# Performance work log

Measured on AMD Instinct MI355X. Metric: run time of the kernel, lower is better.

The kernel has to match this reference:

```python
import jax, jax.numpy as jnp
import numpy as np

N = 50000
E = 800000
D = 128
EPS = 1e-5


def setup_inputs() -> dict:
    key = jax.random.key(0)
    ks = jax.random.split(key, 8)
    scale = 1.0 / np.sqrt(D)
    x = jax.random.normal(ks[0], (N, D), dtype=jnp.float32)
    edge_index = jax.random.randint(ks[1], (2, E), 0, N, dtype=jnp.int64)
    return {
        "x": x,
        "edge_index": edge_index,
        "W1l": jax.random.normal(ks[2], (D, D), dtype=jnp.float32) * scale,
        "b1": jnp.zeros((D,), jnp.float32),
        "W1r": jax.random.normal(ks[3], (D, D), dtype=jnp.float32) * scale,
        "g1": jnp.ones((D,), jnp.float32),
        "bt1": jnp.zeros((D,), jnp.float32),
        "W2l": jax.random.normal(ks[4], (D, D), dtype=jnp.float32) * scale,
        "b2": jnp.zeros((D,), jnp.float32),
        "W2r": jax.random.normal(ks[5], (D, D), dtype=jnp.float32) * scale,
        "g2": jnp.ones((D,), jnp.float32),
        "bt2": jnp.zeros((D,), jnp.float32),
    }


def _sage(x, src, dst, Wl, b, Wr):
    # mean aggregation of source features at destination nodes
    agg = jax.ops.segment_sum(x[src], dst, num_segments=N)  # [N, D]
    deg = jax.ops.segment_sum(jnp.ones((E,), x.dtype), dst, num_segments=N)
    agg = agg / jnp.maximum(deg, 1.0)[:, None]
    # PyG SAGEConv: lin_l(agg) + bias + lin_r(x) (root, no bias)
    return agg @ Wl + b + x @ Wr


def _bn(h, g, bt):
    # training-mode batch norm over node dim
    mu = jnp.mean(h, axis=0)
    var = jnp.var(h, axis=0)
    return (h - mu) * (g / jnp.sqrt(var + EPS)) + bt


def reference(x, edge_index, W1l, b1, W1r, g1, bt1, W2l, b2, W2r, g2, bt2):
    src, dst = edge_index[0], edge_index[1]
    h = _sage(x, src, dst, W1l, b1, W1r)
    h = jax.nn.relu(_bn(h, g1, bt1))
    # dropout = identity (eval mode)
    h = _sage(h, src, dst, W2l, b2, W2r)
    h = _bn(h, g2, bt2)
    # residual (in_channels == out_channels -> identity skip)
    return jax.nn.relu(h + x)
```

## Files before the change

### kernel.cpp

```cpp
#include <hip/hip_runtime.h>

typedef unsigned short u16;
typedef unsigned char u8;
typedef __attribute__((ext_vector_type(8))) short short8;
typedef __attribute__((ext_vector_type(2))) float f32x2;
typedef __attribute__((ext_vector_type(4))) float f32x4;
typedef __attribute__((ext_vector_type(4))) int i32x4;
typedef __attribute__((ext_vector_type(2))) int i32x2;
typedef __attribute__((ext_vector_type(4))) unsigned short us4;
typedef __attribute__((ext_vector_type(8))) unsigned short us8;
typedef __attribute__((ext_vector_type(4))) unsigned int u32x4;

#define N_NODES 50000
#define N_EDGES 800000
#define DIM 128
#define NINV (1.0f / 50000.0f)
#define SROW 136
#define NBKT 3125
#define CAP 512
#define SUPN 800
#define NSUP 63
#define SEGCAP 16384

__device__ __forceinline__ float bf2f(u16 u) {
    union { unsigned int i; float f; } v; v.i = ((unsigned int)u) << 16; return v.f;
}
__device__ __forceinline__ u16 f2bf(float f) {
    union { float f; unsigned int i; } v; v.f = f;
    return (u16)((v.i + 0x7FFFu + ((v.i >> 16) & 1u)) >> 16);
}

__global__ __launch_bounds__(256) void k_prep(
        const float* __restrict__ W1l, const float* __restrict__ W1r, u16* __restrict__ Bp1,
        const float* __restrict__ W2l, const float* __restrict__ W2r, u16* __restrict__ Bp2,
        const float* __restrict__ x, u16* __restrict__ xh, u8* __restrict__ xf8,
        const int* __restrict__ esrc, const int* __restrict__ edst,
        int* __restrict__ segCnt, unsigned* __restrict__ segBuf, int splitB) {
    int b = blockIdx.x;
    if (b < 32) {
        const float* Wl = (b < 16) ? W1l : W2l;
        const float* Wr = (b < 16) ? W1r : W2r;
        u16* Bp = (b < 16) ? Bp1 : Bp2;
        int idx = (b & 15) * 256 + threadIdx.x;
        int lane = idx & 63;
        int kc = (idx >> 6) & 7;
        int nt = idx >> 9;
        int q = lane >> 4, nn = lane & 15;
        int col = nt * 16 + nn;
        #pragma unroll
        for (int j = 0; j < 8; ++j) {
            int k = kc * 32 + q * 8 + j;
            float v = (k < 128) ? Wl[k * 128 + col] : Wr[(k - 128) * 128 + col];
            Bp[(long)idx * 8 + j] = f2bf(v);
        }
    } else if (b < 32 + splitB) {
        long i4 = ((long)(b - 32) * 256 + threadIdx.x) * 4;
        f32x4 v = *(const f32x4*)(x + i4);
        us4 h;
        #pragma unroll
        for (int j = 0; j < 4; ++j) h[j] = f2bf(v[j]);
        *(us4*)(xh + i4) = h;
        int p = __builtin_amdgcn_cvt_pk_fp8_f32(v[0], v[1], 0, false);
        p = __builtin_amdgcn_cvt_pk_fp8_f32(v[2], v[3], p, true);
        *(int*)(xf8 + i4) = p;
    } else {
        __shared__ int sHistB[64], sScanB[64], sCurB[64], sBaseB[64];
        __shared__ unsigned sStage[1024];
        __shared__ u8 sBinOf[1024];
        int tid = threadIdx.x;
        int hb = b - 32 - splitB;
        int e4 = hb * 1024 + tid * 4;
        bool val = e4 < N_EDGES;
        if (tid < 64) sHistB[tid] = 0;
        __syncthreads();
        unsigned ent[4]; int bin[4];
        if (val) {
            i32x4 d4 = *(const i32x4*)(edst + e4);
            i32x4 s4 = *(const i32x4*)(esrc + e4);
            #pragma unroll
            for (int j = 0; j < 4; ++j) {
                unsigned dd = (unsigned)d4[j];
                int bi = (int)(dd / 800u);
                bin[j] = bi;
                ent[j] = ((unsigned)s4[j] << 10) | (dd - (unsigned)bi * 800u);
                atomicAdd(&sHistB[bi], 1);
            }
        }
        __syncthreads();
        if (tid == 0) {
            int acc = 0;
            #pragma unroll
            for (int i = 0; i < 64; ++i) { sScanB[i] = acc; sCurB[i] = acc; acc += sHistB[i]; }
        }
        __syncthreads();
        if (val) {
            #pragma unroll
            for (int j = 0; j < 4; ++j) {
                int p = atomicAdd(&sCurB[bin[j]], 1);
                sStage[p] = ent[j];
                sBinOf[p] = (u8)bin[j];
            }
        }
        __syncthreads();
        if (tid < 64) {
            int c = sHistB[tid];
            sBaseB[tid] = c ? atomicAdd(&segCnt[tid << 4], c) : 0;
        }
        __syncthreads();
        int tcount = sScanB[63] + sHistB[63];
        for (int p = tid; p < tcount; p += 256) {
            int bn = sBinOf[p];
            long ofs = (long)sBaseB[bn] + (p - sScanB[bn]);
            if (ofs < SEGCAP)
                segBuf[(long)bn * SEGCAP + ofs] = sStage[p];
        }
    }
}

__global__ __launch_bounds__(512) void k_sort(
        const int* __restrict__ segCnt, const unsigned* __restrict__ segBuf,
        u16* __restrict__ col_srt, u16* __restrict__ hdr) {
    __shared__ int sHist[SUPN], sStart[SUPN], sCur[SUPN];
    int tid = threadIdx.x;
    int s = blockIdx.x;
    int nnodes = N_NODES - s * SUPN; if (nnodes > SUPN) nnodes = SUPN;
    int ngroups = nnodes >> 4;
    int n = segCnt[s << 4]; if (n > SEGCAP) n = SEGCAP;
    for (int i = tid; i < SUPN; i += 512) { sHist[i] = 0; sCur[i] = 0; }
    __syncthreads();
    const unsigned* seg = segBuf + (long)s * SEGCAP;
    unsigned ent[32];
    #pragma unroll
    for (int i = 0; i < 32; ++i) {
        int idx = i * 512 + tid;
        ent[i] = (idx < n) ? seg[idx] : 0xFFFFFFFFu;
    }
    #pragma unroll
    for (int i = 0; i < 32; ++i)
        if (ent[i] != 0xFFFFFFFFu) atomicAdd(&sHist[ent[i] & 1023u], 1);
    __syncthreads();
    if (tid < ngroups) {
        int base = 0;
        int gb = (s * 50 + tid) * 32;
        #pragma unroll
        for (int i = 0; i < 16; ++i) {
            int node = tid * 16 + i;
            int d = sHist[node];
            int st_c = base < CAP ? base : CAP;
            int en_c = base + d < CAP ? base + d : CAP;
            sStart[node] = base;
            hdr[gb + i] = (u16)st_c;
            hdr[gb + 16 + i] = (u16)(en_c - st_c);
            base += d;
        }
    }
    __syncthreads();
    #pragma unroll
    for (int i = 0; i < 32; ++i) {
        unsigned e = ent[i];
        if (e != 0xFFFFFFFFu) {
            int node = (int)(e & 1023u);
            int pos = atomicAdd(&sCur[node], 1);
            int ofs = sStart[node] + pos;
            if (ofs < CAP)
                col_srt[(long)(s * 50 + (node >> 4)) * CAP + ofs] = (u16)(e >> 10);
        }
    }
}

template<int BN>
__device__ __forceinline__ void acc_row16(u32x4 w,
        f32x2 sum2[8], const f32x2 av2[8], const f32x2 ov2[8]) {
    #pragma unroll
    for (int h = 0; h < 4; ++h) {
        f32x2 lo = __builtin_amdgcn_cvt_pk_f32_fp8((int)w[h], false);
        f32x2 hi = __builtin_amdgcn_cvt_pk_f32_fp8((int)w[h], true);
        if (BN) {
            lo = lo * av2[2 * h] + ov2[2 * h];
            hi = hi * av2[2 * h + 1] + ov2[2 * h + 1];
            lo[0] = lo[0] > 0.f ? lo[0] : 0.f;
            lo[1] = lo[1] > 0.f ? lo[1] : 0.f;
            hi[0] = hi[0] > 0.f ? hi[0] : 0.f;
            hi[1] = hi[1] > 0.f ? hi[1] : 0.f;
        }
        sum2[2 * h]     += lo;
        sum2[2 * h + 1] += hi;
    }
}

template<int BN, int W8>
__global__ __launch_bounds__(256) void k_ag(
        const u8* __restrict__ fq, const u16* __restrict__ fh,
        const u16* __restrict__ hdr, const u16* __restrict__ col_srt,
        const u16* __restrict__ Bph, const float* __restrict__ bias,
        const float* __restrict__ statsPrev, const float* __restrict__ gP,
        const float* __restrict__ btP,
        u16* __restrict__ h16, u8* __restrict__ h8, float* __restrict__ stats) {
    __shared__ u16 sA[16 * SROW];
    __shared__ float acS[256];
    __shared__ __align__(16) u16 sIdx[CAP];
    int tid = threadIdx.x;
    long nodebase = (long)blockIdx.x * 16;

    if (tid < 64)
        *(us8*)(sIdx + tid * 8) = *(const us8*)(col_srt + (long)blockIdx.x * CAP + tid * 8);

    if (BN) {
        if (tid < 128) {
            float s = 0.f, qq = 0.f;
            #pragma unroll
            for (int b = 0; b < 8; ++b) {
                s  += statsPrev[b * 512 + tid];
                qq += statsPrev[b * 512 + 256 + tid];
            }
            float mu = s * NINV;
            float var = qq * NINV - mu * mu;
            float a = gP[tid] * rsqrtf(var + 1e-5f);
            acS[tid] = a;
            acS[128 + tid] = btP[tid] - mu * a;
        }
    }
    __syncthreads();

    {
        int grp = tid >> 4;
        int g   = tid & 15;
        int sub = g >> 3;
        int gl  = g & 7;
        int d16 = gl * 16;
        int st  = hdr[blockIdx.x * 32 + grp];
        int deg = hdr[blockIdx.x * 32 + 16 + grp];
        int s = st, e = st + deg;
        f32x2 av2[8], ov2[8];
        if (BN) {
            #pragma unroll
            for (int p = 0; p < 8; ++p) {
                av2[p] = *(const f32x2*)(acS + d16 + 2 * p);
                ov2[p] = *(const f32x2*)(acS + 128 + d16 + 2 * p);
            }
        }
        f32x2 sum2[8];
        #pragma unroll
        for (int p = 0; p < 8; ++p) sum2[p] = (f32x2){0.f, 0.f};
        int j = s + sub;
        for (; j + 6 < e; j += 8) {
            int i0 = sIdx[j], i1 = sIdx[j + 2], i2 = sIdx[j + 4], i3 = sIdx[j + 6];
            u32x4 w0 = *(const u32x4*)(fq + (long)i0 * DIM + d16);
            u32x4 w1 = *(const u32x4*)(fq + (long)i1 * DIM + d16);
            u32x4 w2 = *(const u32x4*)(fq + (long)i2 * DIM + d16);
            u32x4 w3 = *(const u32x4*)(fq + (long)i3 * DIM + d16);
            acc_row16<BN>(w0, sum2, av2, ov2);
            acc_row16<BN>(w1, sum2, av2, ov2);
            acc_row16<BN>(w2, sum2, av2, ov2);
            acc_row16<BN>(w3, sum2, av2, ov2);
        }
        for (; j < e; j += 2) {
            int i0 = sIdx[j];
            u32x4 w0 = *(const u32x4*)(fq + (long)i0 * DIM + d16);
            acc_row16<BN>(w0, sum2, av2, ov2);
        }
        #pragma unroll
        for (int p = 0; p < 8; ++p) {
            sum2[p][0] += __shfl_xor(sum2[p][0], 8);
            sum2[p][1] += __shfl_xor(sum2[p][1], 8);
        }
        if (sub == 0) {
            float dn = (deg > 0) ? 1.f / (float)deg : 1.f;
            us8 r0, r1;
            #pragma unroll
            for (int k = 0; k < 8; ++k) {
                r0[k] = f2bf(sum2[k >> 1][k & 1] * dn);
                r1[k] = f2bf(sum2[4 + (k >> 1)][k & 1] * dn);
            }
            *(us8*)(sA + grp * SROW + d16) = r0;
            *(us8*)(sA + grp * SROW + d16 + 8) = r1;
        }
    }
    __syncthreads();

    int cg = tid >> 6, lane = tid & 63;
    int q = lane >> 4, nn = lane & 15;
    long rc = nodebase + nn;

    short8 ah[8];
    #pragma unroll
    for (int kc = 0; kc < 4; ++kc)
        ah[kc] = *(const short8*)(sA + nn * SROW + kc * 32 + q * 8);
    #pragma unroll
    for (int kc = 0; kc < 4; ++kc) {
        int ko = kc * 32 + q * 8;
        us8 rv = *(const us8*)(fh + rc * DIM + ko);
        short8 t;
        if (BN) {
            #pragma unroll
            for (int j = 0; j < 8; ++j) {
                float v = bf2f(rv[j]) * acS[ko + j] + acS[128 + ko + j];
                t[j] = (short)f2bf(v > 0.f ? v : 0.f);
            }
        } else {
            #pragma unroll
            for (int j = 0; j < 8; ++j) t[j] = (short)rv[j];
        }
        ah[4 + kc] = t;
    }

    f32x4 acc[2];
    acc[0] = (f32x4){0.f, 0.f, 0.f, 0.f};
    acc[1] = (f32x4){0.f, 0.f, 0.f, 0.f};

    #pragma unroll
    for (int kc = 0; kc < 8; ++kc) {
        #pragma unroll
        for (int nt = 0; nt < 2; ++nt) {
            int ntg = cg * 2 + nt;
            short8 bh = *(const short8*)(Bph + (((ntg * 8 + kc) * 64 + lane) << 3));
            acc[nt] = __builtin_amdgcn_mfma_f32_16x16x32_bf16(ah[kc], bh, acc[nt], 0, 0, 0);
        }
    }

    int bank = blockIdx.x & 7;
    #pragma unroll
    for (int nt = 0; nt < 2; ++nt) {
        int col = cg * 32 + nt * 16 + nn;
        float bv = bias[col];
        float ps = 0.f, pq = 0.f;
        #pragma unroll
        for (int r = 0; r < 4; ++r) {
            float v = acc[nt][r] + bv;
            long idx = (nodebase + q * 4 + r) * DIM + col;
            h16[idx] = f2bf(v);
            if (W8) {
                int pb = __builtin_amdgcn_cvt_pk_fp8_f32(v, v, 0, false);
                h8[idx] = (u8)(pb & 0xff);
            }
            ps += v; pq += v * v;
        }
        ps += __shfl_xor(ps, 16);
        ps += __shfl_xor(ps, 32);
        pq += __shfl_xor(pq, 16);
        pq += __shfl_xor(pq, 32);
        if (q == 0) {
            atomicAdd(&stats[bank * 512 + col], ps);
            atomicAdd(&stats[bank * 512 + 256 + col], pq);
        }
    }
}

__global__ __launch_bounds__(256) void k_bn_add_relu(
        const u16* __restrict__ h, const float* __restrict__ stats,
        const float* __restrict__ g, const float* __restrict__ bt,
        const float* __restrict__ x, float* __restrict__ outv) {
    __shared__ float acS[256];
    int tid = threadIdx.x;
    if (tid < 128) {
        float s = 0.f, qq = 0.f;
        #pragma unroll
        for (int b = 0; b < 8; ++b) {
            s  += stats[b * 512 + tid];
            qq += stats[b * 512 + 256 + tid];
        }
        float mu = s * NINV;
        float var = qq * NINV - mu * mu;
        float a = g[tid] * rsqrtf(var + 1e-5f);
        acS[tid] = a;
        acS[128 + tid] = bt[tid] - mu * a;
    }
    __syncthreads();
    long i8 = ((long)blockIdx.x * 256 + tid) * 8;
    int c = (int)(i8 & 127);
    us8 hv = *(const us8*)(h + i8);
    f32x4 x0 = *(const f32x4*)(x + i8);
    f32x4 x1 = *(const f32x4*)(x + i8 + 4);
    f32x4 r0, r1;
    #pragma unroll
    for (int j = 0; j < 4; ++j) {
        float v = bf2f(hv[j]) * acS[c + j] + acS[128 + c + j] + x0[j];
        r0[j] = v > 0.f ? v : 0.f;
        float w = bf2f(hv[4 + j]) * acS[c + 4 + j] + acS[128 + c + 4 + j] + x1[j];
        r1[j] = w > 0.f ? w : 0.f;
    }
    *(f32x4*)(outv + i8) = r0;
    *(f32x4*)(outv + i8 + 4) = r1;
}

extern "C" void kernel_launch(void* const* d_in, const int* in_sizes, int n_in,
                              void* d_out, int out_size, void* d_ws, size_t ws_size,
                              hipStream_t stream) {
    (void)in_sizes; (void)n_in; (void)out_size; (void)ws_size;
    const float* x   = (const float*)d_in[0];
    const int*   ei  = (const int*)d_in[1];
    const float* W1l = (const float*)d_in[2];
    const float* b1  = (const float*)d_in[3];
    const float* W1r = (const float*)d_in[4];
    const float* g1  = (const float*)d_in[5];
    const float* bt1 = (const float*)d_in[6];
    const float* W2l = (const float*)d_in[7];
    const float* b2  = (const float*)d_in[8];
    const float* W2r = (const float*)d_in[9];
    const float* g2  = (const float*)d_in[10];
    const float* bt2 = (const float*)d_in[11];
    float* out = (float*)d_out;

    const int* esrc = ei;
    const int* edst = ei + N_EDGES;

    char* ws = (char*)d_ws;
    size_t off = 0;
    auto alloc = [&](size_t bytes) { size_t p = off; off = (off + bytes + 255) & ~(size_t)255; return p; };
    float* stats1  = (float*)(ws + alloc(4096 * 4));
    float* stats2  = (float*)(ws + alloc(4096 * 4));
    int*   segCnt  = (int*)  (ws + alloc(64 * 16 * 4));
    size_t zero_bytes = off;
    unsigned* segBuf = (unsigned*)(ws + alloc((size_t)NSUP * SEGCAP * 4));
    u16*   col_srt = (u16*)  (ws + alloc((size_t)NBKT * CAP * 2));
    u16*   hdr     = (u16*)  (ws + alloc((size_t)NBKT * 32 * 2));
    u16*   xh      = (u16*)  (ws + alloc((size_t)N_NODES * DIM * 2));
    u8*    xf8     = (u8*)   (ws + alloc((size_t)N_NODES * DIM));
    u16*   hb1     = (u16*)  (ws + alloc((size_t)N_NODES * DIM * 2));
    u8*    h1f8    = (u8*)   (ws + alloc((size_t)N_NODES * DIM));
    u16*   hb2     = (u16*)  (ws + alloc((size_t)N_NODES * DIM * 2));
    u16*   Bp1h    = (u16*)  (ws + alloc(256 * 128 * 2));
    u16*   Bp2h    = (u16*)  (ws + alloc(256 * 128 * 2));

    hipMemsetAsync(ws, 0, zero_bytes, stream);

    const int AGB = N_NODES / 16;
    const int EWB4 = (int)(((long)N_NODES * DIM) / 1024);
    const int EWB8 = (int)(((long)N_NODES * DIM) / 2048);
    const int EDGB = (N_EDGES + 1023) / 1024;
    const int PREPB = 32 + EWB4 + EDGB;

    k_prep<<<PREPB, 256, 0, stream>>>(W1l, W1r, Bp1h, W2l, W2r, Bp2h, x, xh, xf8,
                                      esrc, edst, segCnt, segBuf, EWB4);

    k_sort<<<NSUP, 512, 0, stream>>>(segCnt, segBuf, col_srt, hdr);

    k_ag<0, 1><<<AGB, 256, 0, stream>>>(xf8, xh, hdr, col_srt, Bp1h, b1,
                                        stats1, g1, bt1, hb1, h1f8, stats1);

    k_ag<1, 0><<<AGB, 256, 0, stream>>>(h1f8, hb1, hdr, col_srt, Bp2h, b2,
                                        stats1, g1, bt1, hb2, h1f8, stats2);

    k_bn_add_relu<<<EWB8, 256, 0, stream>>>(hb2, stats2, g2, bt2, x, out);
}
```

Measured before the change: 205.7 us.

## Split layer-1 BN+ReLU into separate activation kernel before second aggregation

Instead of applying the layer-1 batch-norm affine and ReLU inside the second aggregation's gather loop (once per edge) and on the root features, a new elementwise kernel normalizes hb1 once per node and writes bf16 and fp8 copies. Both aggregation launches then use one simple template-free kernel whose gather loop only converts and sums fp8 values. This removes per-edge FMA/max work at the cost of an extra launch and an additional read/write pass over the node features (about 12.8MB read plus 19.2MB written). The first aggregation also no longer writes the fp8 copy of h1.

```diff
diff --git a/kernel.cpp b/kernel.cpp
--- a/kernel.cpp
+++ b/kernel.cpp
@@ -168,58 +168,26 @@
     }
 }
 
-template<int BN>
-__device__ __forceinline__ void acc_row16(u32x4 w,
-        f32x2 sum2[8], const f32x2 av2[8], const f32x2 ov2[8]) {
+__device__ __forceinline__ void acc_row16(u32x4 w, f32x2 sum2[8]) {
     #pragma unroll
     for (int h = 0; h < 4; ++h) {
-        f32x2 lo = __builtin_amdgcn_cvt_pk_f32_fp8((int)w[h], false);
-        f32x2 hi = __builtin_amdgcn_cvt_pk_f32_fp8((int)w[h], true);
-        if (BN) {
-            lo = lo * av2[2 * h] + ov2[2 * h];
-            hi = hi * av2[2 * h + 1] + ov2[2 * h + 1];
-            lo[0] = lo[0] > 0.f ? lo[0] : 0.f;
-            lo[1] = lo[1] > 0.f ? lo[1] : 0.f;
-            hi[0] = hi[0] > 0.f ? hi[0] : 0.f;
-            hi[1] = hi[1] > 0.f ? hi[1] : 0.f;
-        }
-        sum2[2 * h]     += lo;
-        sum2[2 * h + 1] += hi;
-    }
-}
-
-template<int BN, int W8>
+        sum2[2 * h]     += __builtin_amdgcn_cvt_pk_f32_fp8((int)w[h], false);
+        sum2[2 * h + 1] += __builtin_amdgcn_cvt_pk_f32_fp8((int)w[h], true);
+    }
+}
+
 __global__ __launch_bounds__(256) void k_ag(
         const u8* __restrict__ fq, const u16* __restrict__ fh,
         const u16* __restrict__ hdr, const u16* __restrict__ col_srt,
         const u16* __restrict__ Bph, const float* __restrict__ bias,
-        const float* __restrict__ statsPrev, const float* __restrict__ gP,
-        const float* __restrict__ btP,
-        u16* __restrict__ h16, u8* __restrict__ h8, float* __restrict__ stats) {
+        u16* __restrict__ h16, float* __restrict__ stats) {
     __shared__ u16 sA[16 * SROW];
-    __shared__ float acS[256];
     __shared__ __align__(16) u16 sIdx[CAP];
     int tid = threadIdx.x;
     long nodebase = (long)blockIdx.x * 16;
 
     if (tid < 64)
         *(us8*)(sIdx + tid * 8) = *(const us8*)(col_srt + (long)blockIdx.x * CAP + tid * 8);
-
-    if (BN) {
-        if (tid < 128) {
-            float s = 0.f, qq = 0.f;
-            #pragma unroll
-            for (int b = 0; b < 8; ++b) {
-                s  += statsPrev[b * 512 + tid];
-                qq += statsPrev[b * 512 + 256 + tid];
-            }
-            float mu = s * NINV;
-            float var = qq * NINV - mu * mu;
-            float a = gP[tid] * rsqrtf(var + 1e-5f);
-            acS[tid] = a;
-            acS[128 + tid] = btP[tid] - mu * a;
-        }
-    }
     __syncthreads();
 
     {
@@ -231,14 +199,6 @@
         int st  = hdr[blockIdx.x * 32 + grp];
         int deg = hdr[blockIdx.x * 32 + 16 + grp];
         int s = st, e = st + deg;
-        f32x2 av2[8], ov2[8];
-        if (BN) {
-            #pragma unroll
-            for (int p = 0; p < 8; ++p) {
-                av2[p] = *(const f32x2*)(acS + d16 + 2 * p);
-                ov2[p] = *(const f32x2*)(acS + 128 + d16 + 2 * p);
-            }
-        }
         f32x2 sum2[8];
         #pragma unroll
         for (int p = 0; p < 8; ++p) sum2[p] = (f32x2){0.f, 0.f};
@@ -249,15 +209,15 @@
             u32x4 w1 = *(const u32x4*)(fq + (long)i1 * DIM + d16);
             u32x4 w2 = *(const u32x4*)(fq + (long)i2 * DIM + d16);
             u32x4 w3 = *(const u32x4*)(fq + (long)i3 * DIM + d16);
-            acc_row16<BN>(w0, sum2, av2, ov2);
-            acc_row16<BN>(w1, sum2, av2, ov2);
-            acc_row16<BN>(w2, sum2, av2, ov2);
-            acc_row16<BN>(w3, sum2, av2, ov2);
+            acc_row16(w0, sum2);
+            acc_row16(w1, sum2);
+            acc_row16(w2, sum2);
+            acc_row16(w3, sum2);
         }
         for (; j < e; j += 2) {
             int i0 = sIdx[j];
             u32x4 w0 = *(const u32x4*)(fq + (long)i0 * DIM + d16);
-            acc_row16<BN>(w0, sum2, av2, ov2);
+            acc_row16(w0, sum2);
         }
         #pragma unroll
         for (int p = 0; p < 8; ++p) {
@@ -291,16 +251,8 @@
         int ko = kc * 32 + q * 8;
         us8 rv = *(const us8*)(fh + rc * DIM + ko);
         short8 t;
-        if (BN) {
-            #pragma unroll
-            for (int j = 0; j < 8; ++j) {
-                float v = bf2f(rv[j]) * acS[ko + j] + acS[128 + ko + j];
-                t[j] = (short)f2bf(v > 0.f ? v : 0.f);
-            }
-        } else {
-            #pragma unroll
-            for (int j = 0; j < 8; ++j) t[j] = (short)rv[j];
-        }
+        #pragma unroll
+        for (int j = 0; j < 8; ++j) t[j] = (short)rv[j];
         ah[4 + kc] = t;
     }
 
@@ -329,10 +281,6 @@
             float v = acc[nt][r] + bv;
             long idx = (nodebase + q * 4 + r) * DIM + col;
             h16[idx] = f2bf(v);
-            if (W8) {
-                int pb = __builtin_amdgcn_cvt_pk_fp8_f32(v, v, 0, false);
-                h8[idx] = (u8)(pb & 0xff);
-            }
             ps += v; pq += v * v;
         }
         ps += __shfl_xor(ps, 16);
@@ -344,6 +292,47 @@
             atomicAdd(&stats[bank * 512 + 256 + col], pq);
         }
     }
+}
+
+__global__ __launch_bounds__(256) void k_act(
+        const u16* __restrict__ h, const float* __restrict__ stats,
+        const float* __restrict__ g, const float* __restrict__ bt,
+        u16* __restrict__ outh, u8* __restrict__ outq) {
+    __shared__ float acS[256];
+    int tid = threadIdx.x;
+    if (tid < 128) {
+        float s = 0.f, qq = 0.f;
+        #pragma unroll
+        for (int b = 0; b < 8; ++b) {
+            s  += stats[b * 512 + tid];
+            qq += stats[b * 512 + 256 + tid];
+        }
+        float mu = s * NINV;
+        float var = qq * NINV - mu * mu;
+        float a = g[tid] * rsqrtf(var + 1e-5f);
+        acS[tid] = a;
+        acS[128 + tid] = bt[tid] - mu * a;
+    }
+    __syncthreads();
+    long i8 = ((long)blockIdx.x * 256 + tid) * 8;
+    int c = (int)(i8 & 127);
+    us8 hv = *(const us8*)(h + i8);
+    us8 r;
+    float v[8];
+    #pragma unroll
+    for (int j = 0; j < 8; ++j) {
+        float t = bf2f(hv[j]) * acS[c + j] + acS[128 + c + j];
+        t = t > 0.f ? t : 0.f;
+        v[j] = t;
+        r[j] = f2bf(t);
+    }
+    *(us8*)(outh + i8) = r;
+    int p0 = __builtin_amdgcn_cvt_pk_fp8_f32(v[0], v[1], 0, false);
+    p0 = __builtin_amdgcn_cvt_pk_fp8_f32(v[2], v[3], p0, true);
+    int p1 = __builtin_amdgcn_cvt_pk_fp8_f32(v[4], v[5], 0, false);
+    p1 = __builtin_amdgcn_cvt_pk_fp8_f32(v[6], v[7], p1, true);
+    i32x2 pp; pp[0] = p0; pp[1] = p1;
+    *(i32x2*)(outq + i8) = pp;
 }
 
 __global__ __launch_bounds__(256) void k_bn_add_relu(
@@ -417,7 +406,8 @@
     u16*   xh      = (u16*)  (ws + alloc((size_t)N_NODES * DIM * 2));
     u8*    xf8     = (u8*)   (ws + alloc((size_t)N_NODES * DIM));
     u16*   hb1     = (u16*)  (ws + alloc((size_t)N_NODES * DIM * 2));
-    u8*    h1f8    = (u8*)   (ws + alloc((size_t)N_NODES * DIM));
+    u16*   hah     = (u16*)  (ws + alloc((size_t)N_NODES * DIM * 2));
+    u8*    haf8    = (u8*)   (ws + alloc((size_t)N_NODES * DIM));
     u16*   hb2     = (u16*)  (ws + alloc((size_t)N_NODES * DIM * 2));
     u16*   Bp1h    = (u16*)  (ws + alloc(256 * 128 * 2));
     u16*   Bp2h    = (u16*)  (ws + alloc(256 * 128 * 2));
@@ -435,11 +425,11 @@
 
     k_sort<<<NSUP, 512, 0, stream>>>(segCnt, segBuf, col_srt, hdr);
 
-    k_ag<0, 1><<<AGB, 256, 0, stream>>>(xf8, xh, hdr, col_srt, Bp1h, b1,
-                                        stats1, g1, bt1, hb1, h1f8, stats1);
-
-    k_ag<1, 0><<<AGB, 256, 0, stream>>>(h1f8, hb1, hdr, col_srt, Bp2h, b2,
-                                        stats1, g1, bt1, hb2, h1f8, stats2);
+    k_ag<<<AGB, 256, 0, stream>>>(xf8, xh, hdr, col_srt, Bp1h, b1, hb1, stats1);
+
+    k_act<<<EWB8, 256, 0, stream>>>(hb1, stats1, g1, bt1, hah, haf8);
+
+    k_ag<<<AGB, 256, 0, stream>>>(haf8, hah, hdr, col_srt, Bp2h, b2, hb2, stats2);
 
     k_bn_add_relu<<<EWB8, 256, 0, stream>>>(hb2, stats2, g2, bt2, x, out);
 }
```

Result: no change. 204.7 us (-0.5%).
